# Kernel tuning notes

Measured on AMD Instinct MI355X. Metric: run time of the kernel, lower is better.

## Reference

```python
import jax, jax.numpy as jnp
import numpy as np

N_NODES = 100000
N_EDGES = 600000
HIDDEN = 128
N_LAYERS = 4
ALPHA = 0.1


def setup_inputs() -> dict:
    key = jax.random.key(0)
    ks = jax.random.split(key, 8)
    x = jax.random.normal(ks[0], (N_NODES, HIDDEN), dtype=jnp.float32)
    src = jax.random.randint(ks[1], (N_EDGES,), 0, N_NODES, dtype=jnp.int32)
    dst = jax.random.randint(ks[2], (N_EDGES,), 0, N_NODES, dtype=jnp.int32)
    w = jax.random.uniform(ks[3], (N_EDGES,), dtype=jnp.float32)
    # per-layer GCN linear weights (stored as [in, out]) and biases
    scale = 1.0 / np.sqrt(HIDDEN)
    Ws = jax.random.normal(ks[4], (N_LAYERS, HIDDEN, HIDDEN), dtype=jnp.float32) * scale
    bs = jnp.zeros((N_LAYERS, HIDDEN), dtype=jnp.float32)
    # energy heads: Linear(hidden, 1) for each of num_layers+1 taps
    We = jax.random.normal(ks[5], (N_LAYERS + 1, HIDDEN), dtype=jnp.float32) * scale
    be = jnp.zeros((N_LAYERS + 1,), dtype=jnp.float32)
    # GPR combination weights: alpha*(1-alpha)^k, last = (1-alpha)^L
    t = ALPHA * (1.0 - ALPHA) ** np.arange(N_LAYERS + 1)
    t[-1] = (1.0 - ALPHA) ** N_LAYERS
    temp = jnp.asarray(t, dtype=jnp.float32)
    return {"x": x, "src": src, "dst": dst, "w": w,
            "Ws": Ws, "bs": bs, "We": We, "be": be, "temp": temp}


def reference(x, src, dst, w, Ws, bs, We, be, temp):
    # eval mode: both dropouts are identity
    def gcn_conv(h, W, b):
        h = h @ W + b                      # [N, d] dense projection
        msg = h[src] * w[:, None]          # gather + edge-weight scale [E, d]
        return jax.ops.segment_sum(msg, dst, num_segments=N_NODES)  # scatter-sum

    energy = (x @ We[0] + be[0])[:, None] * temp[0]   # [N, 1]
    for i in range(N_LAYERS):
        x = gcn_conv(x, Ws[i], bs[i])
        x = jax.nn.leaky_relu(x, negative_slope=0.01)
        energy = energy + (x @ We[i + 1] + be[i + 1])[:, None] * temp[i + 1]
    return energy, x
```

## Files before the change

### kernel.cpp

```cpp
#include <hip/hip_runtime.h>
#include <hip/hip_bf16.h>

#define N_NODES 100000
#define N_EDGES 600000
#define HIDDEN 128
#define N_LAYERS 4
#define MPAD 100096

#define TAP0_BLOCKS ((N_NODES * 16) / 256)
#define CNT_BLOCKS ((N_EDGES + 255) / 256)
#define PREPW_BLOCKS ((N_LAYERS * HIDDEN * HIDDEN + 255) / 256)

typedef short bf16x8 __attribute__((ext_vector_type(8)));
typedef float f32x4 __attribute__((ext_vector_type(4)));
typedef float f32x8 __attribute__((ext_vector_type(8)));

__device__ inline ushort f2bf(float f) {
    __hip_bfloat16 h = __float2bfloat16(f);
    return *reinterpret_cast<ushort*>(&h);
}

__device__ inline float bfhi(uint u) { return __uint_as_float(u << 16); }
__device__ inline float bflo(uint u) { return __uint_as_float(u & 0xffff0000u); }

__global__ void prologue(const float* __restrict__ x, const float* __restrict__ We,
                         const float* __restrict__ be, const float* __restrict__ temp,
                         float* __restrict__ energy, uint* __restrict__ xb,
                         const int* __restrict__ dst, int* __restrict__ cnt,
                         const float* __restrict__ Ws, ushort* __restrict__ whi,
                         ushort* __restrict__ wlo) {
    int b = blockIdx.x;
    if (b < TAP0_BLOCKS) {
        int gtid = b * 256 + threadIdx.x;
        int n = gtid >> 4, l16 = gtid & 15;
        f32x8 v = *(const f32x8*)(x + (size_t)n * HIDDEN + l16 * 8);
        uint4 packed;
        packed.x = (uint)f2bf(v[0]) | ((uint)f2bf(v[1]) << 16);
        packed.y = (uint)f2bf(v[2]) | ((uint)f2bf(v[3]) << 16);
        packed.z = (uint)f2bf(v[4]) | ((uint)f2bf(v[5]) << 16);
        packed.w = (uint)f2bf(v[6]) | ((uint)f2bf(v[7]) << 16);
        ((uint4*)(xb + (size_t)n * 64))[l16] = packed;
        f32x8 we = *(const f32x8*)(We + l16 * 8);
        float dot = v[0] * we[0] + v[1] * we[1] + v[2] * we[2] + v[3] * we[3]
                  + v[4] * we[4] + v[5] * we[5] + v[6] * we[6] + v[7] * we[7];
        #pragma unroll
        for (int off = 8; off > 0; off >>= 1) dot += __shfl_xor(dot, off);
        if (l16 == 0) energy[n] = (dot + be[0]) * temp[0];
    } else if (b < TAP0_BLOCKS + CNT_BLOCKS) {
        int e = (b - TAP0_BLOCKS) * 256 + threadIdx.x;
        if (e < N_EDGES) atomicAdd(&cnt[dst[e]], 1);
    } else {
        int idx = (b - TAP0_BLOCKS - CNT_BLOCKS) * 256 + threadIdx.x;
        if (idx < N_LAYERS * HIDDEN * HIDDEN) {
            int l = idx >> 14;
            int r = idx & 16383;
            int c = r >> 7, k = r & 127;
            float v = Ws[(l << 14) + k * HIDDEN + c];
            ushort hi = f2bf(v);
            float hif = __uint_as_float(((uint)hi) << 16);
            whi[idx] = hi;
            wlo[idx] = f2bf(v - hif);
        }
    }
}

__global__ void scan1(const int* __restrict__ cnt, int* __restrict__ excl,
                      int* __restrict__ bsums, int n) {
    __shared__ int lds[8];
    int t = threadIdx.x;
    int base = blockIdx.x * 1024 + t * 4;
    int v0 = (base + 0 < n) ? cnt[base + 0] : 0;
    int v1 = (base + 1 < n) ? cnt[base + 1] : 0;
    int v2 = (base + 2 < n) ? cnt[base + 2] : 0;
    int v3 = (base + 3 < n) ? cnt[base + 3] : 0;
    int tsum = v0 + v1 + v2 + v3;
    int lane = t & 63, wv = t >> 6;
    int s = tsum;
    #pragma unroll
    for (int off = 1; off < 64; off <<= 1) {
        int u = __shfl_up(s, off);
        if (lane >= off) s += u;
    }
    if (lane == 63) lds[wv] = s;
    __syncthreads();
    if (t == 0) {
        int a = 0;
        #pragma unroll
        for (int i = 0; i < 4; ++i) { int bb = lds[i]; lds[i] = a; a += bb; }
        lds[4] = a;
    }
    __syncthreads();
    int excl_t = (s - tsum) + lds[wv];
    if (base + 0 < n) excl[base + 0] = excl_t;
    if (base + 1 < n) excl[base + 1] = excl_t + v0;
    if (base + 2 < n) excl[base + 2] = excl_t + v0 + v1;
    if (base + 3 < n) excl[base + 3] = excl_t + v0 + v1 + v2;
    if (t == 0) bsums[blockIdx.x] = lds[4];
}

__global__ void scan23(const int* __restrict__ excl, const int* __restrict__ bsums,
                       int* __restrict__ rowptr, int n, int nb) {
    __shared__ int bp[128];
    int t = threadIdx.x;
    if (t < nb) bp[t] = bsums[t];
    __syncthreads();
    if (t == 0) {
        int a = 0;
        for (int i = 0; i < nb; ++i) { int v = bp[i]; bp[i] = a; a += v; }
    }
    __syncthreads();
    int i = blockIdx.x * blockDim.x + t;
    if (i < n) rowptr[i] = excl[i] + bp[i >> 10];
    else if (i == n) rowptr[n] = N_EDGES;
}

__global__ void fill_csr(const int* __restrict__ src, const int* __restrict__ dst,
                         const float* __restrict__ w, const int* __restrict__ rowptr,
                         int* __restrict__ fillc, int2* __restrict__ epack) {
    int e = blockIdx.x * blockDim.x + threadIdx.x;
    if (e >= N_EDGES) return;
    int d = dst[e];
    int pos = atomicAdd(&fillc[d], 1);
    int slot = rowptr[d] + pos;
    epack[slot] = make_int2(src[e], __float_as_int(w[e]));
}

__global__ __launch_bounds__(256) void gemm_lds(
    const uint* __restrict__ xb,
    const ushort* __restrict__ whi, const ushort* __restrict__ wlo,
    const float* __restrict__ b, ushort* __restrict__ h) {
    __shared__ uint4 sx4[1024];
    char* sxb = (char*)sx4;
    int t = threadIdx.x;
    int lane = t & 63, wv = t >> 6;
    int l15 = lane & 15, l4 = lane >> 4;
    int row0 = blockIdx.x * 64;
    int c0 = wv * 32;

    bf16x8 Ah[2][4], Al[2][4];
    #pragma unroll
    for (int m = 0; m < 2; ++m) {
        int c = c0 + m * 16 + l15;
        #pragma unroll
        for (int s = 0; s < 4; ++s) {
            int off = c * HIDDEN + s * 32 + l4 * 8;
            Ah[m][s] = *(const bf16x8*)(whi + off);
            Al[m][s] = *(const bf16x8*)(wlo + off);
        }
    }

    #pragma unroll
    for (int j = 0; j < 4; ++j) {
        int c = j * 256 + t;
        int row = c >> 4;
        int colb = (c & 15) * 16;
        int grow = row0 + row;
        if (grow >= N_NODES) grow = N_NODES - 1;
        uint4 v = *(const uint4*)((const char*)xb + (size_t)grow * 256 + colb);
        *(uint4*)(sxb + row * 256 + (colb ^ ((row & 7) << 4))) = v;
    }
    __syncthreads();

    f32x4 acc[2][4];
    #pragma unroll
    for (int m = 0; m < 2; ++m)
        #pragma unroll
        for (int n = 0; n < 4; ++n)
            acc[m][n] = f32x4{0.f, 0.f, 0.f, 0.f};

    #pragma unroll
    for (int n = 0; n < 4; ++n) {
        int row = n * 16 + l15;
        int rsw = (row & 7) << 4;
        #pragma unroll
        for (int s = 0; s < 4; ++s) {
            bf16x8 bh = *(const bf16x8*)(sxb + row * 256 + ((s * 64 + l4 * 16) ^ rsw));
            #pragma unroll
            for (int m = 0; m < 2; ++m) {
                acc[m][n] = __builtin_amdgcn_mfma_f32_16x16x32_bf16(Ah[m][s], bh, acc[m][n], 0, 0, 0);
                acc[m][n] = __builtin_amdgcn_mfma_f32_16x16x32_bf16(Al[m][s], bh, acc[m][n], 0, 0, 0);
            }
        }
    }

    #pragma unroll
    for (int m = 0; m < 2; ++m) {
        f32x4 bias = *(const f32x4*)(b + c0 + m * 16 + l4 * 4);
        #pragma unroll
        for (int n = 0; n < 4; ++n) {
            int node = row0 + n * 16 + l15;
            f32x4 r = acc[m][n] + bias;
            uint2 packed;
            packed.x = (uint)f2bf(r[0]) | ((uint)f2bf(r[1]) << 16);
            packed.y = (uint)f2bf(r[2]) | ((uint)f2bf(r[3]) << 16);
            *(uint2*)(h + (size_t)node * HIDDEN + c0 + m * 16 + l4 * 4) = packed;
        }
    }
}

template <int LAST>
__global__ void agg_relu_tap(const ushort* __restrict__ h, const int* __restrict__ rowptr,
                             const int2* __restrict__ epack,
                             const float* __restrict__ We_l, const float* __restrict__ be_l,
                             const float* __restrict__ temp_l,
                             uint* __restrict__ xb, float* __restrict__ xout,
                             float* __restrict__ energy) {
    int gtid = blockIdx.x * blockDim.x + threadIdx.x;
    int n = gtid >> 4;
    int l16 = gtid & 15;
    if (n >= N_NODES) return;
    int j0 = rowptr[n], j1 = rowptr[n + 1];

    float a0 = 0.f, a1 = 0.f, a2 = 0.f, a3 = 0.f;
    float a4 = 0.f, a5 = 0.f, a6 = 0.f, a7 = 0.f;
    const char* hrow = (const char*)h;
    int cb = l16 * 16;

    int j = j0;
    for (; j + 4 <= j1; j += 4) {
        int2 p0 = epack[j], p1 = epack[j + 1], p2 = epack[j + 2], p3 = epack[j + 3];
        uint4 u0 = *(const uint4*)(hrow + (size_t)p0.x * 256 + cb);
        uint4 u1 = *(const uint4*)(hrow + (size_t)p1.x * 256 + cb);
        uint4 u2 = *(const uint4*)(hrow + (size_t)p2.x * 256 + cb);
        uint4 u3 = *(const uint4*)(hrow + (size_t)p3.x * 256 + cb);
        float w0 = __int_as_float(p0.y), w1 = __int_as_float(p1.y);
        float w2 = __int_as_float(p2.y), w3 = __int_as_float(p3.y);
        a0 += bfhi(u0.x) * w0 + bfhi(u1.x) * w1 + bfhi(u2.x) * w2 + bfhi(u3.x) * w3;
        a1 += bflo(u0.x) * w0 + bflo(u1.x) * w1 + bflo(u2.x) * w2 + bflo(u3.x) * w3;
        a2 += bfhi(u0.y) * w0 + bfhi(u1.y) * w1 + bfhi(u2.y) * w2 + bfhi(u3.y) * w3;
        a3 += bflo(u0.y) * w0 + bflo(u1.y) * w1 + bflo(u2.y) * w2 + bflo(u3.y) * w3;
        a4 += bfhi(u0.z) * w0 + bfhi(u1.z) * w1 + bfhi(u2.z) * w2 + bfhi(u3.z) * w3;
        a5 += bflo(u0.z) * w0 + bflo(u1.z) * w1 + bflo(u2.z) * w2 + bflo(u3.z) * w3;
        a6 += bfhi(u0.w) * w0 + bfhi(u1.w) * w1 + bfhi(u2.w) * w2 + bfhi(u3.w) * w3;
        a7 += bflo(u0.w) * w0 + bflo(u1.w) * w1 + bflo(u2.w) * w2 + bflo(u3.w) * w3;
    }
    if (j + 2 <= j1) {
        int2 p0 = epack[j], p1 = epack[j + 1];
        uint4 u0 = *(const uint4*)(hrow + (size_t)p0.x * 256 + cb);
        uint4 u1 = *(const uint4*)(hrow + (size_t)p1.x * 256 + cb);
        float w0 = __int_as_float(p0.y), w1 = __int_as_float(p1.y);
        a0 += bfhi(u0.x) * w0 + bfhi(u1.x) * w1;
        a1 += bflo(u0.x) * w0 + bflo(u1.x) * w1;
        a2 += bfhi(u0.y) * w0 + bfhi(u1.y) * w1;
        a3 += bflo(u0.y) * w0 + bflo(u1.y) * w1;
        a4 += bfhi(u0.z) * w0 + bfhi(u1.z) * w1;
        a5 += bflo(u0.z) * w0 + bflo(u1.z) * w1;
        a6 += bfhi(u0.w) * w0 + bfhi(u1.w) * w1;
        a7 += bflo(u0.w) * w0 + bflo(u1.w) * w1;
        j += 2;
    }
    if (j < j1) {
        int2 p0 = epack[j];
        uint4 u0 = *(const uint4*)(hrow + (size_t)p0.x * 256 + cb);
        float w0 = __int_as_float(p0.y);
        a0 += bfhi(u0.x) * w0;
        a1 += bflo(u0.x) * w0;
        a2 += bfhi(u0.y) * w0;
        a3 += bflo(u0.y) * w0;
        a4 += bfhi(u0.z) * w0;
        a5 += bflo(u0.z) * w0;
        a6 += bfhi(u0.w) * w0;
        a7 += bflo(u0.w) * w0;
    }

    a0 = a0 > 0.f ? a0 : 0.01f * a0;
    a1 = a1 > 0.f ? a1 : 0.01f * a1;
    a2 = a2 > 0.f ? a2 : 0.01f * a2;
    a3 = a3 > 0.f ? a3 : 0.01f * a3;
    a4 = a4 > 0.f ? a4 : 0.01f * a4;
    a5 = a5 > 0.f ? a5 : 0.01f * a5;
    a6 = a6 > 0.f ? a6 : 0.01f * a6;
    a7 = a7 > 0.f ? a7 : 0.01f * a7;

    if (LAST) {
        float* orow = xout + (size_t)n * HIDDEN + l16 * 8;
        *(float4*)(orow + 0) = float4{a0, a1, a2, a3};
        *(float4*)(orow + 4) = float4{a4, a5, a6, a7};
    } else {
        uint4 packed;
        packed.x = (uint)f2bf(a0) | ((uint)f2bf(a1) << 16);
        packed.y = (uint)f2bf(a2) | ((uint)f2bf(a3) << 16);
        packed.z = (uint)f2bf(a4) | ((uint)f2bf(a5) << 16);
        packed.w = (uint)f2bf(a6) | ((uint)f2bf(a7) << 16);
        ((uint4*)(xb + (size_t)n * 64))[l16] = packed;
    }

    const float* wer = We_l + l16 * 8;
    float4 we0 = *(const float4*)(wer + 0);
    float4 we1 = *(const float4*)(wer + 4);
    float dot = a0 * we0.x + a1 * we0.y + a2 * we0.z + a3 * we0.w
              + a4 * we1.x + a5 * we1.y + a6 * we1.z + a7 * we1.w;
    #pragma unroll
    for (int off = 8; off > 0; off >>= 1) dot += __shfl_xor(dot, off);
    if (l16 == 0) energy[n] += (dot + be_l[0]) * temp_l[0];
}

extern "C" void kernel_launch(void* const* d_in, const int* in_sizes, int n_in,
                              void* d_out, int out_size, void* d_ws, size_t ws_size,
                              hipStream_t stream) {
    const float* x    = (const float*)d_in[0];
    const int*   src  = (const int*)d_in[1];
    const int*   dst  = (const int*)d_in[2];
    const float* w    = (const float*)d_in[3];
    const float* Ws   = (const float*)d_in[4];
    const float* bs   = (const float*)d_in[5];
    const float* We   = (const float*)d_in[6];
    const float* be   = (const float*)d_in[7];
    const float* temp = (const float*)d_in[8];

    float* energy = (float*)d_out;
    float* xout   = (float*)d_out + N_NODES;
    uint* xb = (uint*)xout;

    ushort* h      = (ushort*)d_ws;
    int2*   epack  = (int2*)(h + (size_t)MPAD * HIDDEN);
    int*    cnt    = (int*)(epack + N_EDGES);
    int*    fillc  = cnt + N_NODES;
    int*    excl   = fillc + N_NODES;
    int*    bsums  = excl + N_NODES;
    int*    rowptr = bsums + 128;
    ushort* whi    = (ushort*)(rowptr + N_NODES + 4);
    ushort* wlo    = whi + N_LAYERS * HIDDEN * HIDDEN;

    hipMemsetAsync(cnt, 0, 2 * N_NODES * sizeof(int), stream);

    prologue<<<TAP0_BLOCKS + CNT_BLOCKS + PREPW_BLOCKS, 256, 0, stream>>>(
        x, We, be, temp, energy, xb, dst, cnt, Ws, whi, wlo);

    int nblk = (N_NODES + 1023) / 1024;
    scan1<<<nblk, 256, 0, stream>>>(cnt, excl, bsums, N_NODES);
    scan23<<<(N_NODES + 1 + 255) / 256, 256, 0, stream>>>(excl, bsums, rowptr, N_NODES, nblk);
    fill_csr<<<(N_EDGES + 255) / 256, 256, 0, stream>>>(src, dst, w, rowptr, fillc, epack);

    int agg_blocks = (N_NODES * 16 + 255) / 256;
    for (int i = 0; i < N_LAYERS; ++i) {
        gemm_lds<<<(MPAD / 64), 256, 0, stream>>>(
            xb, whi + (size_t)i * HIDDEN * HIDDEN,
            wlo + (size_t)i * HIDDEN * HIDDEN, bs + (size_t)i * HIDDEN, h);
        if (i < N_LAYERS - 1) {
            agg_relu_tap<0><<<agg_blocks, 256, 0, stream>>>(
                h, rowptr, epack, We + (size_t)(i + 1) * HIDDEN, be + (i + 1),
                temp + (i + 1), xb, xout, energy);
        } else {
            agg_relu_tap<1><<<agg_blocks, 256, 0, stream>>>(
                h, rowptr, epack, We + (size_t)(i + 1) * HIDDEN, be + (i + 1),
                temp + (i + 1), xb, xout, energy);
        }
    }
}
```

Measured before the change: 298.1 us.

## Fuse aggregation with next-layer GEMM and merge CSR fill into first GEMM

Each middle layer's gather-aggregate, leaky ReLU and energy tap now runs in the same kernel as the next layer's MFMA projection. The aggregated rows stay in swizzled LDS as bf16 instead of going to global memory and being read back, and two ping-pong h buffers replace the single one. The CSR fill is folded into the first GEMM launch as extra blocks, so there are fewer launches and less global traffic. The cost is that each fused block serially gathers 64 nodes before its GEMM, with fewer threads per node and lower occupancy for the latency-bound gather.

```diff
diff --git a/kernel.cpp b/kernel.cpp
--- a/kernel.cpp
+++ b/kernel.cpp
@@ -10,6 +10,7 @@
 #define TAP0_BLOCKS ((N_NODES * 16) / 256)
 #define CNT_BLOCKS ((N_EDGES + 255) / 256)
 #define PREPW_BLOCKS ((N_LAYERS * HIDDEN * HIDDEN + 255) / 256)
+#define GEMM_BLOCKS (MPAD / 64)
 
 typedef short bf16x8 __attribute__((ext_vector_type(8)));
 typedef float f32x4 __attribute__((ext_vector_type(4)));
@@ -22,6 +23,38 @@
 
 __device__ inline float bfhi(uint u) { return __uint_as_float(u << 16); }
 __device__ inline float bflo(uint u) { return __uint_as_float(u & 0xffff0000u); }
+
+#define FMA8(U, P) { float wk = __int_as_float(P.y); \
+    a[0] += bfhi(U.x) * wk; a[1] += bflo(U.x) * wk; \
+    a[2] += bfhi(U.y) * wk; a[3] += bflo(U.y) * wk; \
+    a[4] += bfhi(U.z) * wk; a[5] += bflo(U.z) * wk; \
+    a[6] += bfhi(U.w) * wk; a[7] += bflo(U.w) * wk; }
+
+__device__ __forceinline__ void gather_agg(const char* __restrict__ hrow,
+                                           const int2* __restrict__ epack,
+                                           int j0, int j1, int cb, float* a) {
+    int j = j0;
+    for (; j + 4 <= j1; j += 4) {
+        int2 p0 = epack[j], p1 = epack[j + 1], p2 = epack[j + 2], p3 = epack[j + 3];
+        uint4 u0 = *(const uint4*)(hrow + (size_t)p0.x * 256 + cb);
+        uint4 u1 = *(const uint4*)(hrow + (size_t)p1.x * 256 + cb);
+        uint4 u2 = *(const uint4*)(hrow + (size_t)p2.x * 256 + cb);
+        uint4 u3 = *(const uint4*)(hrow + (size_t)p3.x * 256 + cb);
+        FMA8(u0, p0); FMA8(u1, p1); FMA8(u2, p2); FMA8(u3, p3);
+    }
+    if (j + 2 <= j1) {
+        int2 p0 = epack[j], p1 = epack[j + 1];
+        uint4 u0 = *(const uint4*)(hrow + (size_t)p0.x * 256 + cb);
+        uint4 u1 = *(const uint4*)(hrow + (size_t)p1.x * 256 + cb);
+        FMA8(u0, p0); FMA8(u1, p1);
+        j += 2;
+    }
+    if (j < j1) {
+        int2 p0 = epack[j];
+        uint4 u0 = *(const uint4*)(hrow + (size_t)p0.x * 256 + cb);
+        FMA8(u0, p0);
+    }
+}
 
 __global__ void prologue(const float* __restrict__ x, const float* __restrict__ We,
                          const float* __restrict__ be, const float* __restrict__ temp,
@@ -114,24 +147,25 @@
     else if (i == n) rowptr[n] = N_EDGES;
 }
 
-__global__ void fill_csr(const int* __restrict__ src, const int* __restrict__ dst,
-                         const float* __restrict__ w, const int* __restrict__ rowptr,
-                         int* __restrict__ fillc, int2* __restrict__ epack) {
-    int e = blockIdx.x * blockDim.x + threadIdx.x;
-    if (e >= N_EDGES) return;
-    int d = dst[e];
-    int pos = atomicAdd(&fillc[d], 1);
-    int slot = rowptr[d] + pos;
-    epack[slot] = make_int2(src[e], __float_as_int(w[e]));
-}
-
-__global__ __launch_bounds__(256) void gemm_lds(
+__global__ __launch_bounds__(256) void fill_gemm0(
+    const int* __restrict__ src, const int* __restrict__ dst,
+    const float* __restrict__ w, const int* __restrict__ rowptr,
+    int* __restrict__ fillc, int2* __restrict__ epack,
     const uint* __restrict__ xb,
     const ushort* __restrict__ whi, const ushort* __restrict__ wlo,
     const float* __restrict__ b, ushort* __restrict__ h) {
+    int t = threadIdx.x;
+    if (blockIdx.x >= GEMM_BLOCKS) {
+        int e = (blockIdx.x - GEMM_BLOCKS) * 256 + t;
+        if (e < N_EDGES) {
+            int d = dst[e];
+            int pos = atomicAdd(&fillc[d], 1);
+            epack[rowptr[d] + pos] = make_int2(src[e], __float_as_int(w[e]));
+        }
+        return;
+    }
     __shared__ uint4 sx4[1024];
     char* sxb = (char*)sx4;
-    int t = threadIdx.x;
     int lane = t & 63, wv = t >> 6;
     int l15 = lane & 15, l4 = lane >> 4;
     int row0 = blockIdx.x * 64;
@@ -198,98 +232,126 @@
     }
 }
 
-template <int LAST>
-__global__ void agg_relu_tap(const ushort* __restrict__ h, const int* __restrict__ rowptr,
-                             const int2* __restrict__ epack,
-                             const float* __restrict__ We_l, const float* __restrict__ be_l,
-                             const float* __restrict__ temp_l,
-                             uint* __restrict__ xb, float* __restrict__ xout,
-                             float* __restrict__ energy) {
+__global__ __launch_bounds__(256) void agg_gemm(
+    const ushort* __restrict__ hprev, const int* __restrict__ rowptr,
+    const int2* __restrict__ epack,
+    const float* __restrict__ We_l, const float* __restrict__ be_l,
+    const float* __restrict__ temp_l, float* __restrict__ energy,
+    const ushort* __restrict__ whi, const ushort* __restrict__ wlo,
+    const float* __restrict__ b, ushort* __restrict__ hnext) {
+    __shared__ uint4 sx4[1024];
+    char* sxb = (char*)sx4;
+    int t = threadIdx.x;
+    int row0 = blockIdx.x * 64;
+    int g = t >> 4, l16 = t & 15;
+    int cb = l16 * 16;
+    const char* hrow = (const char*)hprev;
+
+    #pragma unroll 1
+    for (int p = 0; p < 4; ++p) {
+        int n = row0 + p * 16 + g;
+        float a[8] = {0.f, 0.f, 0.f, 0.f, 0.f, 0.f, 0.f, 0.f};
+        if (n < N_NODES) {
+            int j0 = rowptr[n], j1 = rowptr[n + 1];
+            gather_agg(hrow, epack, j0, j1, cb, a);
+            #pragma unroll
+            for (int q = 0; q < 8; ++q) a[q] = a[q] > 0.f ? a[q] : 0.01f * a[q];
+            const float* wer = We_l + l16 * 8;
+            float4 we0 = *(const float4*)(wer + 0);
+            float4 we1 = *(const float4*)(wer + 4);
+            float dot = a[0] * we0.x + a[1] * we0.y + a[2] * we0.z + a[3] * we0.w
+                      + a[4] * we1.x + a[5] * we1.y + a[6] * we1.z + a[7] * we1.w;
+            #pragma unroll
+            for (int off = 8; off > 0; off >>= 1) dot += __shfl_xor(dot, off);
+            if (l16 == 0) energy[n] += (dot + be_l[0]) * temp_l[0];
+        }
+        uint4 packed;
+        packed.x = (uint)f2bf(a[0]) | ((uint)f2bf(a[1]) << 16);
+        packed.y = (uint)f2bf(a[2]) | ((uint)f2bf(a[3]) << 16);
+        packed.z = (uint)f2bf(a[4]) | ((uint)f2bf(a[5]) << 16);
+        packed.w = (uint)f2bf(a[6]) | ((uint)f2bf(a[7]) << 16);
+        int r = p * 16 + g;
+        *(uint4*)(sxb + r * 256 + (cb ^ ((r & 7) << 4))) = packed;
+    }
+
+    int lane = t & 63, wv = t >> 6;
+    int l15 = lane & 15, l4 = lane >> 4;
+    int c0 = wv * 32;
+    bf16x8 Ah[2][4], Al[2][4];
+    #pragma unroll
+    for (int m = 0; m < 2; ++m) {
+        int c = c0 + m * 16 + l15;
+        #pragma unroll
+        for (int s = 0; s < 4; ++s) {
+            int off = c * HIDDEN + s * 32 + l4 * 8;
+            Ah[m][s] = *(const bf16x8*)(whi + off);
+            Al[m][s] = *(const bf16x8*)(wlo + off);
+        }
+    }
+    __syncthreads();
+
+    f32x4 acc[2][4];
+    #pragma unroll
+    for (int m = 0; m < 2; ++m)
+        #pragma unroll
+        for (int n = 0; n < 4; ++n)
+            acc[m][n] = f32x4{0.f, 0.f, 0.f, 0.f};
+
+    #pragma unroll
+    for (int n = 0; n < 4; ++n) {
+        int row = n * 16 + l15;
+        int rsw = (row & 7) << 4;
+        #pragma unroll
+        for (int s = 0; s < 4; ++s) {
+            bf16x8 bh = *(const bf16x8*)(sxb + row * 256 + ((s * 64 + l4 * 16) ^ rsw));
+            #pragma unroll
+            for (int m = 0; m < 2; ++m) {
+                acc[m][n] = __builtin_amdgcn_mfma_f32_16x16x32_bf16(Ah[m][s], bh, acc[m][n], 0, 0, 0);
+                acc[m][n] = __builtin_amdgcn_mfma_f32_16x16x32_bf16(Al[m][s], bh, acc[m][n], 0, 0, 0);
+            }
+        }
+    }
+
+    #pragma unroll
+    for (int m = 0; m < 2; ++m) {
+        f32x4 bias = *(const f32x4*)(b + c0 + m * 16 + l4 * 4);
+        #pragma unroll
+        for (int n = 0; n < 4; ++n) {
+            int node = row0 + n * 16 + l15;
+            f32x4 r = acc[m][n] + bias;
+            uint2 packed;
+            packed.x = (uint)f2bf(r[0]) | ((uint)f2bf(r[1]) << 16);
+            packed.y = (uint)f2bf(r[2]) | ((uint)f2bf(r[3]) << 16);
+            *(uint2*)(hnext + (size_t)node * HIDDEN + c0 + m * 16 + l4 * 4) = packed;
+        }
+    }
+}
+
+__global__ void agg_final(const ushort* __restrict__ h, const int* __restrict__ rowptr,
+                          const int2* __restrict__ epack,
+                          const float* __restrict__ We_l, const float* __restrict__ be_l,
+                          const float* __restrict__ temp_l,
+                          float* __restrict__ xout, float* __restrict__ energy) {
     int gtid = blockIdx.x * blockDim.x + threadIdx.x;
     int n = gtid >> 4;
     int l16 = gtid & 15;
     if (n >= N_NODES) return;
     int j0 = rowptr[n], j1 = rowptr[n + 1];
-
-    float a0 = 0.f, a1 = 0.f, a2 = 0.f, a3 = 0.f;
-    float a4 = 0.f, a5 = 0.f, a6 = 0.f, a7 = 0.f;
-    const char* hrow = (const char*)h;
     int cb = l16 * 16;
-
-    int j = j0;
-    for (; j + 4 <= j1; j += 4) {
-        int2 p0 = epack[j], p1 = epack[j + 1], p2 = epack[j + 2], p3 = epack[j + 3];
-        uint4 u0 = *(const uint4*)(hrow + (size_t)p0.x * 256 + cb);
-        uint4 u1 = *(const uint4*)(hrow + (size_t)p1.x * 256 + cb);
-        uint4 u2 = *(const uint4*)(hrow + (size_t)p2.x * 256 + cb);
-        uint4 u3 = *(const uint4*)(hrow + (size_t)p3.x * 256 + cb);
-        float w0 = __int_as_float(p0.y), w1 = __int_as_float(p1.y);
-        float w2 = __int_as_float(p2.y), w3 = __int_as_float(p3.y);
-        a0 += bfhi(u0.x) * w0 + bfhi(u1.x) * w1 + bfhi(u2.x) * w2 + bfhi(u3.x) * w3;
-        a1 += bflo(u0.x) * w0 + bflo(u1.x) * w1 + bflo(u2.x) * w2 + bflo(u3.x) * w3;
-        a2 += bfhi(u0.y) * w0 + bfhi(u1.y) * w1 + bfhi(u2.y) * w2 + bfhi(u3.y) * w3;
-        a3 += bflo(u0.y) * w0 + bflo(u1.y) * w1 + bflo(u2.y) * w2 + bflo(u3.y) * w3;
-        a4 += bfhi(u0.z) * w0 + bfhi(u1.z) * w1 + bfhi(u2.z) * w2 + bfhi(u3.z) * w3;
-        a5 += bflo(u0.z) * w0 + bflo(u1.z) * w1 + bflo(u2.z) * w2 + bflo(u3.z) * w3;
-        a6 += bfhi(u0.w) * w0 + bfhi(u1.w) * w1 + bfhi(u2.w) * w2 + bfhi(u3.w) * w3;
-        a7 += bflo(u0.w) * w0 + bflo(u1.w) * w1 + bflo(u2.w) * w2 + bflo(u3.w) * w3;
-    }
-    if (j + 2 <= j1) {
-        int2 p0 = epack[j], p1 = epack[j + 1];
-        uint4 u0 = *(const uint4*)(hrow + (size_t)p0.x * 256 + cb);
-        uint4 u1 = *(const uint4*)(hrow + (size_t)p1.x * 256 + cb);
-        float w0 = __int_as_float(p0.y), w1 = __int_as_float(p1.y);
-        a0 += bfhi(u0.x) * w0 + bfhi(u1.x) * w1;
-        a1 += bflo(u0.x) * w0 + bflo(u1.x) * w1;
-        a2 += bfhi(u0.y) * w0 + bfhi(u1.y) * w1;
-        a3 += bflo(u0.y) * w0 + bflo(u1.y) * w1;
-        a4 += bfhi(u0.z) * w0 + bfhi(u1.z) * w1;
-        a5 += bflo(u0.z) * w0 + bflo(u1.z) * w1;
-        a6 += bfhi(u0.w) * w0 + bfhi(u1.w) * w1;
-        a7 += bflo(u0.w) * w0 + bflo(u1.w) * w1;
-        j += 2;
-    }
-    if (j < j1) {
-        int2 p0 = epack[j];
-        uint4 u0 = *(const uint4*)(hrow + (size_t)p0.x * 256 + cb);
-        float w0 = __int_as_float(p0.y);
-        a0 += bfhi(u0.x) * w0;
-        a1 += bflo(u0.x) * w0;
-        a2 += bfhi(u0.y) * w0;
-        a3 += bflo(u0.y) * w0;
-        a4 += bfhi(u0.z) * w0;
-        a5 += bflo(u0.z) * w0;
-        a6 += bfhi(u0.w) * w0;
-        a7 += bflo(u0.w) * w0;
-    }
-
-    a0 = a0 > 0.f ? a0 : 0.01f * a0;
-    a1 = a1 > 0.f ? a1 : 0.01f * a1;
-    a2 = a2 > 0.f ? a2 : 0.01f * a2;
-    a3 = a3 > 0.f ? a3 : 0.01f * a3;
-    a4 = a4 > 0.f ? a4 : 0.01f * a4;
-    a5 = a5 > 0.f ? a5 : 0.01f * a5;
-    a6 = a6 > 0.f ? a6 : 0.01f * a6;
-    a7 = a7 > 0.f ? a7 : 0.01f * a7;
-
-    if (LAST) {
-        float* orow = xout + (size_t)n * HIDDEN + l16 * 8;
-        *(float4*)(orow + 0) = float4{a0, a1, a2, a3};
-        *(float4*)(orow + 4) = float4{a4, a5, a6, a7};
-    } else {
-        uint4 packed;
-        packed.x = (uint)f2bf(a0) | ((uint)f2bf(a1) << 16);
-        packed.y = (uint)f2bf(a2) | ((uint)f2bf(a3) << 16);
-        packed.z = (uint)f2bf(a4) | ((uint)f2bf(a5) << 16);
-        packed.w = (uint)f2bf(a6) | ((uint)f2bf(a7) << 16);
-        ((uint4*)(xb + (size_t)n * 64))[l16] = packed;
-    }
+    float a[8] = {0.f, 0.f, 0.f, 0.f, 0.f, 0.f, 0.f, 0.f};
+    gather_agg((const char*)h, epack, j0, j1, cb, a);
+    #pragma unroll
+    for (int q = 0; q < 8; ++q) a[q] = a[q] > 0.f ? a[q] : 0.01f * a[q];
+
+    float* orow = xout + (size_t)n * HIDDEN + l16 * 8;
+    *(float4*)(orow + 0) = float4{a[0], a[1], a[2], a[3]};
+    *(float4*)(orow + 4) = float4{a[4], a[5], a[6], a[7]};
 
     const float* wer = We_l + l16 * 8;
     float4 we0 = *(const float4*)(wer + 0);
     float4 we1 = *(const float4*)(wer + 4);
-    float dot = a0 * we0.x + a1 * we0.y + a2 * we0.z + a3 * we0.w
-              + a4 * we1.x + a5 * we1.y + a6 * we1.z + a7 * we1.w;
+    float dot = a[0] * we0.x + a[1] * we0.y + a[2] * we0.z + a[3] * we0.w
+              + a[4] * we1.x + a[5] * we1.y + a[6] * we1.z + a[7] * we1.w;
     #pragma unroll
     for (int off = 8; off > 0; off >>= 1) dot += __shfl_xor(dot, off);
     if (l16 == 0) energy[n] += (dot + be_l[0]) * temp_l[0];
@@ -312,8 +374,9 @@
     float* xout   = (float*)d_out + N_NODES;
     uint* xb = (uint*)xout;
 
-    ushort* h      = (ushort*)d_ws;
-    int2*   epack  = (int2*)(h + (size_t)MPAD * HIDDEN);
+    ushort* h0     = (ushort*)d_ws;
+    ushort* h1     = h0 + (size_t)MPAD * HIDDEN;
+    int2*   epack  = (int2*)(h1 + (size_t)MPAD * HIDDEN);
     int*    cnt    = (int*)(epack + N_EDGES);
     int*    fillc  = cnt + N_NODES;
     int*    excl   = fillc + N_NODES;
@@ -330,21 +393,20 @@
     int nblk = (N_NODES + 1023) / 1024;
     scan1<<<nblk, 256, 0, stream>>>(cnt, excl, bsums, N_NODES);
     scan23<<<(N_NODES + 1 + 255) / 256, 256, 0, stream>>>(excl, bsums, rowptr, N_NODES, nblk);
-    fill_csr<<<(N_EDGES + 255) / 256, 256, 0, stream>>>(src, dst, w, rowptr, fillc, epack);
-
-    int agg_blocks = (N_NODES * 16 + 255) / 256;
-    for (int i = 0; i < N_LAYERS; ++i) {
-        gemm_lds<<<(MPAD / 64), 256, 0, stream>>>(
-            xb, whi + (size_t)i * HIDDEN * HIDDEN,
-            wlo + (size_t)i * HIDDEN * HIDDEN, bs + (size_t)i * HIDDEN, h);
-        if (i < N_LAYERS - 1) {
-            agg_relu_tap<0><<<agg_blocks, 256, 0, stream>>>(
-                h, rowptr, epack, We + (size_t)(i + 1) * HIDDEN, be + (i + 1),
-                temp + (i + 1), xb, xout, energy);
-        } else {
-            agg_relu_tap<1><<<agg_blocks, 256, 0, stream>>>(
-                h, rowptr, epack, We + (size_t)(i + 1) * HIDDEN, be + (i + 1),
-                temp + (i + 1), xb, xout, energy);
-        }
-    }
-}
+
+    fill_gemm0<<<GEMM_BLOCKS + CNT_BLOCKS, 256, 0, stream>>>(
+        src, dst, w, rowptr, fillc, epack, xb, whi, wlo, bs, h0);
+
+    agg_gemm<<<GEMM_BLOCKS, 256, 0, stream>>>(
+        h0, rowptr, epack, We + 1 * HIDDEN, be + 1, temp + 1, energy,
+        whi + 1 * HIDDEN * HIDDEN, wlo + 1 * HIDDEN * HIDDEN, bs + 1 * HIDDEN, h1);
+    agg_gemm<<<GEMM_BLOCKS, 256, 0, stream>>>(
+        h1, rowptr, epack, We + 2 * HIDDEN, be + 2, temp + 2, energy,
+        whi + 2 * HIDDEN * HIDDEN, wlo + 2 * HIDDEN * HIDDEN, bs + 2 * HIDDEN, h0);
+    agg_gemm<<<GEMM_BLOCKS, 256, 0, stream>>>(
+        h0, rowptr, epack, We + 3 * HIDDEN, be + 3, temp + 3, energy,
+        whi + 3 * HIDDEN * HIDDEN, wlo + 3 * HIDDEN * HIDDEN, bs + 3 * HIDDEN, h1);
+
+    agg_final<<<(N_NODES * 16 + 255) / 256, 256, 0, stream>>>(
+        h1, rowptr, epack, We + 4 * HIDDEN, be + 4, temp + 4, xout, energy);
+}
```

New measurement: 289.8 us. 1.03x faster.
